# Kernel optimization log

Measured on AMD Instinct MI355X. Metric: run time of the kernel, lower is better.

The kernel has to match this reference:

```python
import jax, jax.numpy as jnp
import numpy as np

BATCH, N_FEATURES, D_MODEL = 8192, 8192, 1024


def setup_inputs() -> dict:
    key = jax.random.key(0)
    kx, kw = jax.random.split(key)
    # x: sparse feature activations in the original (COO); dense uniform here.
    x = jax.random.uniform(kx, (BATCH, N_FEATURES), dtype=jnp.float32)
    # Xavier-normal init for W_tr [n_features, d_model].
    std = float(np.sqrt(2.0 / (N_FEATURES + D_MODEL)))
    W_tr = jax.random.normal(kw, (N_FEATURES, D_MODEL), dtype=jnp.float32) * std
    bias = jnp.zeros((N_FEATURES,), dtype=jnp.float32)
    return {"x": x, "W_tr": W_tr, "bias": bias}


def reference(x, W_tr, bias):
    # h = x @ W_tr              : [B, n_features] @ [n_features, d_model] -> [B, d_model]
    # out = relu(h @ W_tr.T + b): [B, d_model] @ [d_model, n_features] -> [B, n_features]
    h = jnp.einsum("bf,fd->bd", x, W_tr)
    return jax.nn.relu(jnp.einsum("bd,fd->bf", h, W_tr) + bias)
```

## Files before the change

### kernel.cpp

```cpp
#include <hip/hip_runtime.h>
#include <hip/hip_bf16.h>
#include <stdint.h>

#define BATCH  8192
#define NFEAT  8192
#define DMODEL 1024

typedef unsigned short u16;
typedef __attribute__((ext_vector_type(8))) short  short8;
typedef __attribute__((ext_vector_type(4))) float  f32x4;

__device__ __forceinline__ u16 f2b(float f) {
    uint32_t u = __float_as_uint(f);
    u += 0x7fffu + ((u >> 16) & 1u);
    return (u16)(u >> 16);
}

__device__ __forceinline__ void gld16(const u16* g, void* l) {
    __builtin_amdgcn_global_load_lds(
        (const __attribute__((address_space(1))) void*)(uintptr_t)g,
        (__attribute__((address_space(3))) void*)(uint32_t)(uintptr_t)l,
        16, 0, 0);
}


__global__ void cvt_x_kernel(const float* __restrict__ x, u16* __restrict__ xb) {
    int i = blockIdx.x * blockDim.x + threadIdx.x;
    const float4* xv = (const float4*)x;
    float4 a = xv[2 * i];
    float4 b = xv[2 * i + 1];
    union { u16 u[8]; uint4 v; } o;
    o.u[0] = f2b(a.x); o.u[1] = f2b(a.y); o.u[2] = f2b(a.z); o.u[3] = f2b(a.w);
    o.u[4] = f2b(b.x); o.u[5] = f2b(b.y); o.u[6] = f2b(b.z); o.u[7] = f2b(b.w);
    ((uint4*)xb)[i] = o.v;
}

__global__ void cvt_w_kernel(const float* __restrict__ W,
                             u16* __restrict__ wb, u16* __restrict__ wt) {
    __shared__ u16 tile[64][65];
    const int f0 = blockIdx.x * 64;
    const int d0 = blockIdx.y * 64;
    const int t  = threadIdx.x;
#pragma unroll
    for (int rep = 0; rep < 16; ++rep) {
        int idx = rep * 256 + t;
        int r = idx >> 6, c = idx & 63;
        float v = W[(size_t)(f0 + r) * DMODEL + d0 + c];
        u16 u = f2b(v);
        tile[r][c] = u;
        wb[(size_t)(f0 + r) * DMODEL + d0 + c] = u;
    }
    __syncthreads();
#pragma unroll
    for (int rep = 0; rep < 16; ++rep) {
        int idx = rep * 256 + t;
        int r = idx >> 6, c = idx & 63;
        wt[(size_t)(d0 + r) * NFEAT + f0 + c] = tile[c][r];
    }
}

#define SYNC_IN()  do { __builtin_amdgcn_sched_barrier(0); __builtin_amdgcn_s_barrier(); \
                        asm volatile("s_waitcnt lgkmcnt(0)" ::: "memory");               \
                        __builtin_amdgcn_sched_barrier(0); } while (0)
#define SYNC_OUT() do { __builtin_amdgcn_s_setprio(0); __builtin_amdgcn_sched_barrier(0); \
                        __builtin_amdgcn_s_barrier(); } while (0)

__global__ __launch_bounds__(512, 2)
void gemm1_8phase(const u16* __restrict__ A, const u16* __restrict__ B,
                  u16* __restrict__ H, int N, int K) {
    const int NT = K >> 6;
    __shared__ __align__(1024) char lds[131072];
    const int BOFF = 98304;

    const int tid  = threadIdx.x;
    const int lane = tid & 63;
    const int wave = tid >> 6;
    const int wm   = wave >> 2;
    const int wn   = wave & 3;

    const int nwg = gridDim.x;
    const int swz = (blockIdx.x & 7) * (nwg >> 3) + (blockIdx.x >> 3);
    const int ntn = N >> 7;
    const int tm0 = (swz / ntn) << 8;
    const int tn0 = (swz % ntn) << 7;

    const int srl = lane >> 2;
    const int sch = (lane & 3) ^ (((lane >> 5) & 1) << 1);
    const int scol  = (wave & 1) * 32 + sch * 8;
    const int srow0 = (wave >> 1) * 16 + srl;

    const u16* pa[2][2];
    pa[0][0] = A + (size_t)(tm0 + srow0)            * K + scol;
    pa[0][1] = A + (size_t)(tm0 + srow0 + 64)       * K + scol;
    pa[1][0] = A + (size_t)(tm0 + 128 + srow0)      * K + scol;
    pa[1][1] = A + (size_t)(tm0 + 128 + srow0 + 64) * K + scol;
    const u16* pb[2];
    pb[0] = B + (size_t)(tn0 + srow0)      * K + scol;
    pb[1] = B + (size_t)(tn0 + srow0 + 64) * K + scol;

    auto STAGE_A = [&](int tau, int half) {
        if (tau < NT) {
            char* d = lds + (tau % 3) * 32768 + half * 16384 + wave * 1024;
            gld16(pa[half][0] + (size_t)tau * 64, d);
            gld16(pa[half][1] + (size_t)tau * 64, d + 8192);
        }
    };
    auto STAGE_B = [&](int tau) {
        if (tau < NT) {
            char* d = lds + BOFF + (tau & 1) * 16384 + wave * 1024;
            gld16(pb[0] + (size_t)tau * 64, d);
            gld16(pb[1] + (size_t)tau * 64, d + 8192);
        }
    };

    const int l15 = lane & 15, lhi = lane >> 4;
    const int pch = lhi ^ (((lane >> 3) & 1) << 1);
    const int lof = l15 * 64 + pch * 16;

    short8 a[4][2];
    short8 b[2][2];
    f32x4  acc[8][2] = {};

    const char* Ab;
    const char* Bb;
    auto LDA_ = [&](int mh) {
#pragma unroll
        for (int fm = 0; fm < 4; ++fm)
#pragma unroll
            for (int ks = 0; ks < 2; ++ks)
                a[fm][ks] = *(const short8*)(Ab + ((mh * 4 + fm) * 2 + ks) * 1024);
    };
    auto LDB_ = [&](int nh) {
#pragma unroll
        for (int ks = 0; ks < 2; ++ks)
            b[nh][ks] = *(const short8*)(Bb + (nh * 2 + ks) * 1024);
    };
    auto MMA_ = [&](int mh, int nh) {
#pragma unroll
        for (int ks = 0; ks < 2; ++ks)
#pragma unroll
            for (int fm = 0; fm < 4; ++fm)
                acc[mh * 4 + fm][nh] = __builtin_amdgcn_mfma_f32_16x16x32_bf16(
                    a[fm][ks], b[nh][ks], acc[mh * 4 + fm][nh], 0, 0, 0);
    };

    STAGE_A(0, 0); STAGE_A(0, 1); STAGE_B(0);
    STAGE_A(1, 0); STAGE_A(1, 1); STAGE_B(1);
    asm volatile("s_waitcnt vmcnt(6)" ::: "memory");
    __builtin_amdgcn_s_barrier();

    for (int t = 0; t < NT; ++t) {
        Ab = lds + (t % 3) * 32768 + wm * 16384 + lof;
        Bb = lds + BOFF + (t & 1) * 16384 + wn * 4096 + lof;

        LDA_(0); LDB_(0);
        STAGE_A(t + 2, 0);
        SYNC_IN();
        __builtin_amdgcn_s_setprio(1);
        MMA_(0, 0);
        SYNC_OUT();

        LDB_(1);
        STAGE_A(t + 2, 1);
        SYNC_IN();
        __builtin_amdgcn_s_setprio(1);
        MMA_(0, 1);
        SYNC_OUT();

        LDA_(1);
        STAGE_B(t + 2);
        SYNC_IN();
        __builtin_amdgcn_s_setprio(1);
        MMA_(1, 1);
        SYNC_OUT();

        __builtin_amdgcn_sched_barrier(0);
        __builtin_amdgcn_s_barrier();
        __builtin_amdgcn_s_setprio(1);
        MMA_(1, 0);
        __builtin_amdgcn_s_setprio(0);
        __builtin_amdgcn_sched_barrier(0);
        if (t < NT - 2)       asm volatile("s_waitcnt vmcnt(6)" ::: "memory");
        else if (t == NT - 2) asm volatile("s_waitcnt vmcnt(0)" ::: "memory");
        __builtin_amdgcn_s_barrier();
    }

    u16* lu = (u16*)lds;
#pragma unroll
    for (int fm = 0; fm < 8; ++fm)
#pragma unroll
        for (int nh = 0; nh < 2; ++nh) {
            const int col  = wn * 32 + nh * 16 + l15;
            const int row0 = wm * 128 + fm * 16 + lhi * 4;
#pragma unroll
            for (int r = 0; r < 4; ++r)
                lu[(row0 + r) * 128 + col] = f2b(acc[fm][nh][r]);
        }
    __syncthreads();
    const uint4* ls = (const uint4*)lds;
#pragma unroll
    for (int s = 0; s < 8; ++s) {
        int i = s * 512 + tid;
        int row = i >> 4;
        int col = (i & 15) * 8;
        *(uint4*)(H + (size_t)(tm0 + row) * N + (tn0 + col)) = ls[i];
    }
}

__global__ __launch_bounds__(512, 2)
void gemm2_8phase(const u16* __restrict__ A, const u16* __restrict__ B,
                  float* __restrict__ O, const float* __restrict__ bias,
                  int N, int K) {
    const int NT = K >> 6;
    __shared__ __align__(1024) char lds[163840];
    const int BOFF = 98304;

    const int tid  = threadIdx.x;
    const int lane = tid & 63;
    const int wave = tid >> 6;
    const int wm   = wave >> 2;
    const int wn   = wave & 3;

    const int nwg = gridDim.x;
    const int swz = (blockIdx.x & 7) * (nwg >> 3) + (blockIdx.x >> 3);
    const int ntn = N >> 8;
    const int tm0 = (swz / ntn) << 8;
    const int tn0 = (swz % ntn) << 8;

    const int srl = lane >> 2;
    const int sch = (lane & 3) ^ (((lane >> 5) & 1) << 1);
    const int scol  = (wave & 1) * 32 + sch * 8;
    const int srow0 = (wave >> 1) * 16 + srl;

    const u16* pa[2][2];
    const u16* pb[2][2];
    pa[0][0] = A + (size_t)(tm0 + srow0)       * K + scol;
    pa[0][1] = A + (size_t)(tm0 + srow0 + 64)  * K + scol;
    pa[1][0] = A + (size_t)(tm0 + 128 + srow0)      * K + scol;
    pa[1][1] = A + (size_t)(tm0 + 128 + srow0 + 64) * K + scol;
    pb[0][0] = B + (size_t)(tn0 + srow0)       * K + scol;
    pb[0][1] = B + (size_t)(tn0 + srow0 + 64)  * K + scol;
    pb[1][0] = B + (size_t)(tn0 + 128 + srow0)      * K + scol;
    pb[1][1] = B + (size_t)(tn0 + 128 + srow0 + 64) * K + scol;

    auto STAGE_A = [&](int tau, int half) {
        if (tau < NT) {
            char* d = lds + (tau % 3) * 32768 + half * 16384 + wave * 1024;
            gld16(pa[half][0] + (size_t)tau * 64, d);
            gld16(pa[half][1] + (size_t)tau * 64, d + 8192);
        }
    };
    auto STAGE_B = [&](int tau, int half) {
        if (tau < NT) {
            char* d = lds + BOFF + (tau & 1) * 32768 + half * 16384 + wave * 1024;
            gld16(pb[half][0] + (size_t)tau * 64, d);
            gld16(pb[half][1] + (size_t)tau * 64, d + 8192);
        }
    };

    const int l15 = lane & 15, lhi = lane >> 4;
    const int pch = lhi ^ (((lane >> 3) & 1) << 1);
    const int lof = l15 * 64 + pch * 16;

    short8 a[4][2];
    short8 b[4][2];
    f32x4  acc[8][4] = {};

    const char* Ab;
    const char* Bb;
    auto LDA_ = [&](int mh) {
#pragma unroll
        for (int fm = 0; fm < 4; ++fm)
#pragma unroll
            for (int ks = 0; ks < 2; ++ks)
                a[fm][ks] = *(const short8*)(Ab + ((mh * 4 + fm) * 2 + ks) * 1024);
    };
    auto LDB_ = [&](int nh) {
#pragma unroll
        for (int fn = 0; fn < 2; ++fn)
#pragma unroll
            for (int ks = 0; ks < 2; ++ks)
                b[nh * 2 + fn][ks] = *(const short8*)(Bb + (((wn & 1) * 4 + nh * 2 + fn) * 2 + ks) * 1024);
    };
    auto MMA_ = [&](int mh, int nh) {
#pragma unroll
        for (int ks = 0; ks < 2; ++ks)
#pragma unroll
            for (int fm = 0; fm < 4; ++fm)
#pragma unroll
                for (int fn = 0; fn < 2; ++fn)
                    acc[mh * 4 + fm][nh * 2 + fn] = __builtin_amdgcn_mfma_f32_16x16x32_bf16(
                        a[fm][ks], b[nh * 2 + fn][ks], acc[mh * 4 + fm][nh * 2 + fn], 0, 0, 0);
    };

    STAGE_A(0, 0); STAGE_A(0, 1); STAGE_B(0, 0); STAGE_B(0, 1);
    STAGE_A(1, 0); STAGE_A(1, 1); STAGE_B(1, 0); STAGE_B(1, 1);
    asm volatile("s_waitcnt vmcnt(8)" ::: "memory");
    __builtin_amdgcn_s_barrier();

    for (int t = 0; t < NT; ++t) {
        Ab = lds + (t % 3) * 32768 + wm * 16384 + lof;
        Bb = lds + BOFF + (t & 1) * 32768 + (wn >> 1) * 16384 + lof;

        LDA_(0); LDB_(0);
        STAGE_A(t + 2, 0);
        asm volatile("s_waitcnt lgkmcnt(8)" ::: "memory");
        SYNC_IN();
        __builtin_amdgcn_s_setprio(1);
        MMA_(0, 0);
        SYNC_OUT();

        LDB_(1);
        STAGE_A(t + 2, 1);
        SYNC_IN();
        __builtin_amdgcn_s_setprio(1);
        MMA_(0, 1);
        SYNC_OUT();

        LDA_(1);
        STAGE_B(t + 2, 0);
        SYNC_IN();
        __builtin_amdgcn_s_setprio(1);
        MMA_(1, 1);
        SYNC_OUT();

        STAGE_B(t + 2, 1);
        __builtin_amdgcn_sched_barrier(0);
        __builtin_amdgcn_s_barrier();
        asm volatile("s_waitcnt lgkmcnt(0)" ::: "memory");
        __builtin_amdgcn_sched_barrier(0);
        __builtin_amdgcn_s_setprio(1);
        MMA_(1, 0);
        __builtin_amdgcn_s_setprio(0);
        __builtin_amdgcn_sched_barrier(0);
        if (t < NT - 2)       asm volatile("s_waitcnt vmcnt(8)" ::: "memory");
        else if (t == NT - 2) asm volatile("s_waitcnt vmcnt(0)" ::: "memory");
        __builtin_amdgcn_s_barrier();
    }

    const int orow = tm0 + wm * 128;
    const int ocol = tn0 + wn * 64;
    float bv[4];
#pragma unroll
    for (int fn = 0; fn < 4; ++fn) bv[fn] = bias[ocol + fn * 16 + l15];
#pragma unroll
    for (int fm = 0; fm < 8; ++fm) {
        const int row0 = orow + fm * 16 + lhi * 4;
#pragma unroll
        for (int fn = 0; fn < 4; ++fn) {
            const int col = ocol + fn * 16 + l15;
#pragma unroll
            for (int r = 0; r < 4; ++r) {
                float v = acc[fm][fn][r] + bv[fn];
                O[(size_t)(row0 + r) * N + col] = v > 0.f ? v : 0.f;
            }
        }
    }
}


extern "C" void kernel_launch(void* const* d_in, const int* in_sizes, int n_in,
                              void* d_out, int out_size, void* d_ws, size_t ws_size,
                              hipStream_t stream) {
    const float* x    = (const float*)d_in[0];
    const float* W    = (const float*)d_in[1];
    const float* bias = (const float*)d_in[2];
    float* out = (float*)d_out;

    char* ws = (char*)d_ws;
    u16* xb = (u16*)ws;
    u16* wt = (u16*)(ws + 134217728);
    u16* wb = (u16*)(ws + 134217728 + 16777216);
    u16* hb = (u16*)(ws + 134217728 + 2 * 16777216);

    cvt_x_kernel<<<(BATCH * NFEAT / 8) / 256, 256, 0, stream>>>(x, xb);
    cvt_w_kernel<<<dim3(NFEAT / 64, DMODEL / 64), 256, 0, stream>>>(W, wb, wt);

    gemm1_8phase<<<dim3((BATCH / 256) * (DMODEL / 128)), 512, 0, stream>>>(
        xb, wt, hb, DMODEL, NFEAT);

    gemm2_8phase<<<dim3((BATCH / 256) * (NFEAT / 256)), 512, 0, stream>>>(
        hb, wb, out, bias, NFEAT, DMODEL);
}
```

Measured before the change: 384.7 us.

## Fuse fp32-to-bf16 conversion of x into GEMM1 register-staged A loads

Removes the separate cvt_x kernel and has GEMM1 load fp32 x tiles directly into registers, convert them to bf16, and write them to LDS. The A buffer drops from triple-buffered async global-to-LDS loads to double-buffered register staging. This removes a 256MB read plus a 128MB write and re-read of the bf16 copy of x. In exchange GEMM1 reads twice the A bytes per tile, uses more VGPRs, and gives up the direct-to-LDS async copy path, which may hurt overlap.

Result: slower. 447.3 us (+16.3%).

```diff
diff --git a/kernel.cpp b/kernel.cpp
--- a/kernel.cpp
+++ b/kernel.cpp
@@ -23,17 +23,6 @@
         16, 0, 0);
 }
 
-
-__global__ void cvt_x_kernel(const float* __restrict__ x, u16* __restrict__ xb) {
-    int i = blockIdx.x * blockDim.x + threadIdx.x;
-    const float4* xv = (const float4*)x;
-    float4 a = xv[2 * i];
-    float4 b = xv[2 * i + 1];
-    union { u16 u[8]; uint4 v; } o;
-    o.u[0] = f2b(a.x); o.u[1] = f2b(a.y); o.u[2] = f2b(a.z); o.u[3] = f2b(a.w);
-    o.u[4] = f2b(b.x); o.u[5] = f2b(b.y); o.u[6] = f2b(b.z); o.u[7] = f2b(b.w);
-    ((uint4*)xb)[i] = o.v;
-}
 
 __global__ void cvt_w_kernel(const float* __restrict__ W,
                              u16* __restrict__ wb, u16* __restrict__ wt) {
@@ -66,11 +55,11 @@
                         __builtin_amdgcn_s_barrier(); } while (0)
 
 __global__ __launch_bounds__(512, 2)
-void gemm1_8phase(const u16* __restrict__ A, const u16* __restrict__ B,
+void gemm1_8phase(const float* __restrict__ X, const u16* __restrict__ B,
                   u16* __restrict__ H, int N, int K) {
     const int NT = K >> 6;
-    __shared__ __align__(1024) char lds[131072];
-    const int BOFF = 98304;
+    __shared__ __align__(1024) char lds[98304];
+    const int BOFF = 65536;
 
     const int tid  = threadIdx.x;
     const int lane = tid & 63;
@@ -89,21 +78,41 @@
     const int scol  = (wave & 1) * 32 + sch * 8;
     const int srow0 = (wave >> 1) * 16 + srl;
 
-    const u16* pa[2][2];
-    pa[0][0] = A + (size_t)(tm0 + srow0)            * K + scol;
-    pa[0][1] = A + (size_t)(tm0 + srow0 + 64)       * K + scol;
-    pa[1][0] = A + (size_t)(tm0 + 128 + srow0)      * K + scol;
-    pa[1][1] = A + (size_t)(tm0 + 128 + srow0 + 64) * K + scol;
+    const float* px[2][2];
+    px[0][0] = X + (size_t)(tm0 + srow0)            * K + scol;
+    px[0][1] = X + (size_t)(tm0 + srow0 + 64)       * K + scol;
+    px[1][0] = X + (size_t)(tm0 + 128 + srow0)      * K + scol;
+    px[1][1] = X + (size_t)(tm0 + 128 + srow0 + 64) * K + scol;
     const u16* pb[2];
     pb[0] = B + (size_t)(tn0 + srow0)      * K + scol;
     pb[1] = B + (size_t)(tn0 + srow0 + 64) * K + scol;
 
-    auto STAGE_A = [&](int tau, int half) {
-        if (tau < NT) {
-            char* d = lds + (tau % 3) * 32768 + half * 16384 + wave * 1024;
-            gld16(pa[half][0] + (size_t)tau * 64, d);
-            gld16(pa[half][1] + (size_t)tau * 64, d + 8192);
-        }
+    char* const awr = lds + wave * 1024 + lane * 16;
+
+    f32x4 raw[8];
+    auto LOAD_RAW = [&](int tau) {
+#pragma unroll
+        for (int h = 0; h < 2; ++h)
+#pragma unroll
+            for (int j = 0; j < 2; ++j)
+#pragma unroll
+                for (int v = 0; v < 2; ++v)
+                    raw[h * 4 + j * 2 + v] =
+                        *(const f32x4*)(px[h][j] + (size_t)tau * 64 + v * 4);
+    };
+    auto WRITE_A = [&](int buf) {
+#pragma unroll
+        for (int h = 0; h < 2; ++h)
+#pragma unroll
+            for (int j = 0; j < 2; ++j) {
+                union { u16 u[8]; uint4 v; } o;
+#pragma unroll
+                for (int v = 0; v < 2; ++v)
+#pragma unroll
+                    for (int e = 0; e < 4; ++e)
+                        o.u[v * 4 + e] = f2b(raw[h * 4 + j * 2 + v][e]);
+                *(uint4*)(awr + buf * 32768 + h * 16384 + j * 8192) = o.v;
+            }
     };
     auto STAGE_B = [&](int tau) {
         if (tau < NT) {
@@ -144,24 +153,25 @@
                     a[fm][ks], b[nh][ks], acc[mh * 4 + fm][nh], 0, 0, 0);
     };
 
-    STAGE_A(0, 0); STAGE_A(0, 1); STAGE_B(0);
-    STAGE_A(1, 0); STAGE_A(1, 1); STAGE_B(1);
-    asm volatile("s_waitcnt vmcnt(6)" ::: "memory");
+    LOAD_RAW(0);
+    STAGE_B(0); STAGE_B(1);
+    asm volatile("s_waitcnt vmcnt(2)" ::: "memory");
+    WRITE_A(0);
+    asm volatile("s_waitcnt lgkmcnt(0)" ::: "memory");
     __builtin_amdgcn_s_barrier();
 
     for (int t = 0; t < NT; ++t) {
-        Ab = lds + (t % 3) * 32768 + wm * 16384 + lof;
+        Ab = lds + (t & 1) * 32768 + wm * 16384 + lof;
         Bb = lds + BOFF + (t & 1) * 16384 + wn * 4096 + lof;
 
+        if (t + 1 < NT) LOAD_RAW(t + 1);
         LDA_(0); LDB_(0);
-        STAGE_A(t + 2, 0);
         SYNC_IN();
         __builtin_amdgcn_s_setprio(1);
         MMA_(0, 0);
         SYNC_OUT();
 
         LDB_(1);
-        STAGE_A(t + 2, 1);
         SYNC_IN();
         __builtin_amdgcn_s_setprio(1);
         MMA_(0, 1);
@@ -174,14 +184,16 @@
         MMA_(1, 1);
         SYNC_OUT();
 
+        if (t < NT - 2)  asm volatile("s_waitcnt vmcnt(2)" ::: "memory");
+        else             asm volatile("s_waitcnt vmcnt(0)" ::: "memory");
+        if (t + 1 < NT) WRITE_A((t + 1) & 1);
         __builtin_amdgcn_sched_barrier(0);
         __builtin_amdgcn_s_barrier();
         __builtin_amdgcn_s_setprio(1);
         MMA_(1, 0);
         __builtin_amdgcn_s_setprio(0);
-        __builtin_amdgcn_sched_barrier(0);
-        if (t < NT - 2)       asm volatile("s_waitcnt vmcnt(6)" ::: "memory");
-        else if (t == NT - 2) asm volatile("s_waitcnt vmcnt(0)" ::: "memory");
+        asm volatile("s_waitcnt lgkmcnt(0)" ::: "memory");
+        __builtin_amdgcn_sched_barrier(0);
         __builtin_amdgcn_s_barrier();
     }
 
@@ -368,16 +380,14 @@
     float* out = (float*)d_out;
 
     char* ws = (char*)d_ws;
-    u16* xb = (u16*)ws;
-    u16* wt = (u16*)(ws + 134217728);
-    u16* wb = (u16*)(ws + 134217728 + 16777216);
-    u16* hb = (u16*)(ws + 134217728 + 2 * 16777216);
-
-    cvt_x_kernel<<<(BATCH * NFEAT / 8) / 256, 256, 0, stream>>>(x, xb);
+    u16* wt = (u16*)ws;
+    u16* wb = (u16*)(ws + 16777216);
+    u16* hb = (u16*)(ws + 2 * 16777216);
+
     cvt_w_kernel<<<dim3(NFEAT / 64, DMODEL / 64), 256, 0, stream>>>(W, wb, wt);
 
     gemm1_8phase<<<dim3((BATCH / 256) * (DMODEL / 128)), 512, 0, stream>>>(
-        xb, wt, hb, DMODEL, NFEAT);
+        x, wt, hb, DMODEL, NFEAT);
 
     gemm2_8phase<<<dim3((BATCH / 256) * (NFEAT / 256)), 512, 0, stream>>>(
         hb, wb, out, bias, NFEAT, DMODEL);
```
